# Performance work log

Measured on AMD Instinct MI355X. Metric: run time of the kernel, lower is better.

## Reference

```python
import jax, jax.numpy as jnp
import numpy as np
import math

B, C, H, W = 32, 1024, 32, 32
D = 1024  # d == in_channels == H*W (required by the module's own code)


def _conv1x1(x, w, b):
    # x: (B,C,H,W), w: (out,in), b: (out,)
    return jnp.einsum('bchw,dc->bdhw', x, w) + b[None, :, None, None]


def setup_inputs() -> dict:
    key = jax.random.key(0)
    ks = jax.random.split(key, 20)
    s = 0.02
    d = {'x': jax.random.normal(ks[0], (B, C, H, W), dtype=jnp.float32)}
    names = ['w1', 'w2', 'w3', 'w4', 'w5', 'w6', 'w7']
    for i, n in enumerate(names):
        d[n] = s * jax.random.normal(ks[1 + 2 * i], (D, D), dtype=jnp.float32)
        d['b' + n[1:]] = s * jax.random.normal(ks[2 + 2 * i], (D,), dtype=jnp.float32)
    d['wl'] = s * jax.random.normal(ks[16], (D, D), dtype=jnp.float32)
    d['bl'] = s * jax.random.normal(ks[17], (D,), dtype=jnp.float32)
    return d


def reference(x, w1, b1, w2, b2, w3, b3, w4, b4, w5, b5, w6, b6, w7, b7, wl, bl):
    b, c, h, w = x.shape
    d = w1.shape[0]
    n = h * w
    scale = 1.0 / math.sqrt(d)

    def lin(z):  # Linear(d,d) over the LAST dim (= n = d here)
        return jnp.einsum('bdn,mn->bdm', z, wl) + bl

    # --- attention block 1 ---
    Q1 = _conv1x1(x, w1, b1).reshape(b, d, n)
    K1 = _conv1x1(x, w2, b2).reshape(b, d, n)
    V1 = _conv1x1(x, w3, b3).reshape(b, d, n)
    A1 = jax.nn.softmax(jnp.einsum('bdn,bdm->bnm', Q1, K1) * scale, axis=-1)  # (b,n,n)
    O1 = jnp.einsum('bdm,bnm->bdn', V1, A1)  # V1 @ A1^T -> (b,d,n)
    X1 = O1.reshape(b, d, h, w) + x

    # --- attention block 2 ---
    Q2 = lin(_conv1x1(X1, w5, b5).reshape(b, d, n))
    K2 = lin(_conv1x1(X1, w6, b6).reshape(b, d, n))
    V2 = lin(_conv1x1(X1, w7, b7).reshape(b, d, n))
    A2 = jax.nn.softmax(jnp.einsum('bdn,bdm->bnm', Q2, K2) * scale, axis=-1)  # (b,n,n)
    O2 = jnp.einsum('bnm,bkm->bkn', A2, V2)  # (A2 @ V2^T)^T -> (b,d,n)
    X2 = _conv1x1(O2.reshape(b, d, h, w), w4, b4) + X1
    return X2
```

## Files before the change

### kernel.cpp

```cpp
#include <hip/hip_runtime.h>
#include <hip/hip_bf16.h>
#include <cstdint>

typedef unsigned short u16;
typedef __bf16 bf16x8 __attribute__((ext_vector_type(8)));
typedef float f32x4 __attribute__((ext_vector_type(4)));
typedef unsigned short us8 __attribute__((ext_vector_type(8)));

#define AS1 __attribute__((address_space(1)))
#define AS3 __attribute__((address_space(3)))

__device__ __forceinline__ float b2f(u16 u) {
    union { float f; uint32_t i; } c; c.i = ((uint32_t)u) << 16; return c.f;
}
__device__ __forceinline__ u16 f2b(float f) {
    union { float f; uint32_t i; } c; c.f = f;
    return (u16)((c.i + 0x7fffu + ((c.i >> 16) & 1u)) >> 16);
}

#define BM 256
#define BN 256
#define BK 64
#define GK 1024
#define GN 1024
#define NKT (GK / BK)

#define BAR asm volatile("s_barrier" ::: "memory")

template <typename OutT>
__global__ __launch_bounds__(512, 2) void gemm_nt(
    const u16* __restrict__ A, long long sA,
    const u16* __restrict__ B, long long sB,
    OutT* __restrict__ C, long long sC,
    const float* __restrict__ bias, int biasMode,
    const u16* __restrict__ res, long long sR,
    float scale,
    const float* __restrict__ r1u, const float* __restrict__ r1v)
{
    __shared__ __align__(16) char smem[131072];

    const int t = threadIdx.x;
    const int orig = blockIdx.x;
    const int id2 = (orig & 7) * 64 + (orig >> 3);
    const int bz = id2 >> 4;
    const int by = (id2 >> 2) & 3;
    const int bx = id2 & 3;

    const u16* Ab = A + (size_t)bz * sA + (size_t)(by * BM) * GK;
    const u16* Bb = B + (size_t)bz * sB + (size_t)(bx * BN) * GK;

    const int wave = t >> 6, lane = t & 63;
    const int l16 = lane & 15, quad = lane >> 4;
    const int wr = wave >> 2;
    const int wc = wave & 3;
    const int bq = l16 & 7;

    f32x4 acc[8][4] = {};

    int geoff[2], ldoff[2];
    #pragma unroll
    for (int i = 0; i < 2; ++i) {
        const int c = t + 512 * i;
        const int r = c >> 3, js = c & 7;
        geoff[i] = r * GK + (js ^ (r & 7)) * 8;
        ldoff[i] = c * 16;
    }

    #define STG_A(tile, h)                                                               \
        _Pragma("unroll")                                                                \
        for (int i = 0; i < 2; ++i)                                                      \
            __builtin_amdgcn_global_load_lds(                                            \
                (AS1 const void*)(Ab + (size_t)(h) * 128 * GK + geoff[i] + (tile) * BK), \
                (AS3 void*)(smem + ((tile) & 1) * 65536 + (h) * 16384 + ldoff[i]),       \
                16, 0, 0);
    #define STG_B(tile, h)                                                               \
        _Pragma("unroll")                                                                \
        for (int i = 0; i < 2; ++i)                                                      \
            __builtin_amdgcn_global_load_lds(                                            \
                (AS1 const void*)(Bb + (size_t)(h) * 128 * GK + geoff[i] + (tile) * BK), \
                (AS3 void*)(smem + ((tile) & 1) * 65536 + 32768 + (h) * 16384 + ldoff[i]), \
                16, 0, 0);

    auto ldsA = [&](int p, int mh, int mi, int kk) -> const bf16x8* {
        return (const bf16x8*)(smem + p * 65536 + wr * 16384
            + (mh * 64 + mi * 16 + l16) * 128 + (((kk * 4 + quad) ^ bq) * 16));
    };
    auto ldsB = [&](int p, int nh, int ni, int kk) -> const bf16x8* {
        return (const bf16x8*)(smem + p * 65536 + 32768 + (wc >> 1) * 16384
            + ((wc & 1) * 64 + nh * 32 + ni * 16 + l16) * 128 + (((kk * 4 + quad) ^ bq) * 16));
    };

    auto group = [&](int tile) {
        const int p = tile & 1;
        const bool stA = (tile + 1) < NKT;
        const bool stB = (tile + 2) < NKT;
        bf16x8 af[4][2], b0[2][2], b1[2][2];

        #pragma unroll
        for (int mi = 0; mi < 4; ++mi)
            #pragma unroll
            for (int kk = 0; kk < 2; ++kk)
                af[mi][kk] = *ldsA(p, 0, mi, kk);
        #pragma unroll
        for (int ni = 0; ni < 2; ++ni)
            #pragma unroll
            for (int kk = 0; kk < 2; ++kk)
                b0[ni][kk] = *ldsB(p, 0, ni, kk);
        if (stA) { STG_A(tile + 1, 0) }
        BAR;
        __builtin_amdgcn_s_setprio(1);
        #pragma unroll
        for (int kk = 0; kk < 2; ++kk)
            #pragma unroll
            for (int mi = 0; mi < 4; ++mi)
                #pragma unroll
                for (int ni = 0; ni < 2; ++ni)
                    acc[mi][ni] = __builtin_amdgcn_mfma_f32_16x16x32_bf16(af[mi][kk], b0[ni][kk], acc[mi][ni], 0, 0, 0);
        __builtin_amdgcn_s_setprio(0);
        BAR;

        #pragma unroll
        for (int ni = 0; ni < 2; ++ni)
            #pragma unroll
            for (int kk = 0; kk < 2; ++kk)
                b1[ni][kk] = *ldsB(p, 1, ni, kk);
        if (stA) { STG_A(tile + 1, 1) }
        BAR;
        __builtin_amdgcn_s_setprio(1);
        #pragma unroll
        for (int kk = 0; kk < 2; ++kk)
            #pragma unroll
            for (int mi = 0; mi < 4; ++mi)
                #pragma unroll
                for (int ni = 0; ni < 2; ++ni)
                    acc[mi][2 + ni] = __builtin_amdgcn_mfma_f32_16x16x32_bf16(af[mi][kk], b1[ni][kk], acc[mi][2 + ni], 0, 0, 0);
        __builtin_amdgcn_s_setprio(0);
        BAR;

        #pragma unroll
        for (int mi = 0; mi < 4; ++mi)
            #pragma unroll
            for (int kk = 0; kk < 2; ++kk)
                af[mi][kk] = *ldsA(p, 1, mi, kk);
        if (stB) { STG_B(tile + 2, 0) }
        BAR;
        __builtin_amdgcn_s_setprio(1);
        #pragma unroll
        for (int kk = 0; kk < 2; ++kk)
            #pragma unroll
            for (int mi = 0; mi < 4; ++mi)
                #pragma unroll
                for (int ni = 0; ni < 2; ++ni)
                    acc[4 + mi][2 + ni] = __builtin_amdgcn_mfma_f32_16x16x32_bf16(af[mi][kk], b1[ni][kk], acc[4 + mi][2 + ni], 0, 0, 0);
        __builtin_amdgcn_s_setprio(0);
        BAR;

        if (stB) { STG_B(tile + 2, 1) }
        BAR;
        __builtin_amdgcn_s_setprio(1);
        #pragma unroll
        for (int kk = 0; kk < 2; ++kk)
            #pragma unroll
            for (int mi = 0; mi < 4; ++mi)
                #pragma unroll
                for (int ni = 0; ni < 2; ++ni)
                    acc[4 + mi][ni] = __builtin_amdgcn_mfma_f32_16x16x32_bf16(af[mi][kk], b0[ni][kk], acc[4 + mi][ni], 0, 0, 0);
        __builtin_amdgcn_s_setprio(0);
        if (stB) { asm volatile("s_waitcnt vmcnt(4)" ::: "memory"); }
        else     { asm volatile("s_waitcnt vmcnt(0)" ::: "memory"); }
        BAR;
    };

    STG_A(0, 0) STG_A(0, 1) STG_B(0, 0) STG_B(0, 1) STG_B(1, 0) STG_B(1, 1)
    asm volatile("s_waitcnt vmcnt(4)" ::: "memory");
    BAR;

    #pragma unroll 1
    for (int j = 0; j < NKT / 2; ++j) {
        group(2 * j);
        group(2 * j + 1);
    }

    float* Cs = (float*)smem;
    #pragma unroll
    for (int mh = 0; mh < 2; ++mh) {
        __syncthreads();
        if (wr == mh) {
            #pragma unroll
            for (int mi = 0; mi < 8; ++mi)
                #pragma unroll
                for (int ni = 0; ni < 4; ++ni) {
                    const int col = wc * 64 + ni * 16 + l16;
                    const int jc = col >> 2, cw = col & 3;
                    #pragma unroll
                    for (int r2 = 0; r2 < 4; ++r2) {
                        const int row = mi * 16 + quad * 4 + r2;
                        Cs[row * 256 + ((jc ^ (row & 15)) << 2) + cw] = acc[mi][ni][r2];
                    }
                }
        }
        __syncthreads();

        if constexpr (__is_same(OutT, u16)) {
            #pragma unroll
            for (int i = 0; i < 8; ++i) {
                const int c = t + 512 * i;
                const int lr = c >> 5, cc = c & 31;
                const int sxy = lr & 15;
                const float* s0 = Cs + lr * 256 + (((cc * 2) ^ sxy) << 2);
                const float* s1 = Cs + lr * 256 + (((cc * 2 + 1) ^ sxy) << 2);
                float4 a = *(const float4*)s0;
                float4 b = *(const float4*)s1;
                const int grow = by * BM + mh * 128 + lr;
                const int gcol = bx * BN + cc * 8;
                const float br = (biasMode == 1) ? bias[grow] : 0.0f;
                float v[8] = {a.x, a.y, a.z, a.w, b.x, b.y, b.z, b.w};
                #pragma unroll
                for (int jj = 0; jj < 8; ++jj) v[jj] = v[jj] * scale + br;
                if (biasMode == 2) {
                    float4 c1 = *(const float4*)(bias + gcol);
                    float4 c2 = *(const float4*)(bias + gcol + 4);
                    v[0] += c1.x; v[1] += c1.y; v[2] += c1.z; v[3] += c1.w;
                    v[4] += c2.x; v[5] += c2.y; v[6] += c2.z; v[7] += c2.w;
                }
                if (r1u) {
                    const float u = r1u[grow];
                    float4 c1 = *(const float4*)(r1v + gcol);
                    float4 c2 = *(const float4*)(r1v + gcol + 4);
                    v[0] += u * c1.x; v[1] += u * c1.y; v[2] += u * c1.z; v[3] += u * c1.w;
                    v[4] += u * c2.x; v[5] += u * c2.y; v[6] += u * c2.z; v[7] += u * c2.w;
                }
                if (res) {
                    us8 rv = *(const us8*)(res + (size_t)bz * sR + (size_t)grow * GN + gcol);
                    #pragma unroll
                    for (int jj = 0; jj < 8; ++jj) v[jj] += b2f(rv[jj]);
                }
                us8 o;
                #pragma unroll
                for (int jj = 0; jj < 8; ++jj) o[jj] = f2b(v[jj]);
                *(us8*)((u16*)C + (size_t)bz * sC + (size_t)grow * GN + gcol) = o;
            }
        } else {
            #pragma unroll
            for (int i = 0; i < 16; ++i) {
                const int c = t + 512 * i;
                const int lr = c >> 6, cc4 = c & 63;
                const float* src = Cs + lr * 256 + ((cc4 ^ (lr & 15)) << 2);
                float4 a = *(const float4*)src;
                const int grow = by * BM + mh * 128 + lr;
                const int gcol = bx * BN + cc4 * 4;
                const float br = (biasMode == 1) ? bias[grow] : 0.0f;
                float v[4] = {a.x, a.y, a.z, a.w};
                #pragma unroll
                for (int jj = 0; jj < 4; ++jj) v[jj] = v[jj] * scale + br;
                if (biasMode == 2) {
                    float4 c1 = *(const float4*)(bias + gcol);
                    v[0] += c1.x; v[1] += c1.y; v[2] += c1.z; v[3] += c1.w;
                }
                if (r1u) {
                    const float u = r1u[grow];
                    float4 c1 = *(const float4*)(r1v + gcol);
                    v[0] += u * c1.x; v[1] += u * c1.y; v[2] += u * c1.z; v[3] += u * c1.w;
                }
                if (res) {
                    ushort4 rv = *(const ushort4*)(res + (size_t)bz * sR + (size_t)grow * GN + gcol);
                    v[0] += b2f(rv.x); v[1] += b2f(rv.y); v[2] += b2f(rv.z); v[3] += b2f(rv.w);
                }
                float4 o = {v[0], v[1], v[2], v[3]};
                *(float4*)((float*)C + (size_t)bz * sC + (size_t)grow * GN + gcol) = o;
            }
        }
    }
    #undef STG_A
    #undef STG_B
}

__global__ __launch_bounds__(256) void softmax_rows(u16* __restrict__ S)
{
    const size_t row = blockIdx.x;
    u16* p = S + row * 1024;
    const int t = threadIdx.x;
    ushort4 u = ((const ushort4*)p)[t];
    float v0 = b2f(u.x), v1 = b2f(u.y), v2 = b2f(u.z), v3 = b2f(u.w);

    float m = fmaxf(fmaxf(v0, v1), fmaxf(v2, v3));
    #pragma unroll
    for (int o = 32; o > 0; o >>= 1) m = fmaxf(m, __shfl_xor(m, o, 64));
    __shared__ float red[8];
    const int wave = t >> 6, lane = t & 63;
    if (lane == 0) red[wave] = m;
    __syncthreads();
    m = fmaxf(fmaxf(red[0], red[1]), fmaxf(red[2], red[3]));

    v0 = __expf(v0 - m); v1 = __expf(v1 - m); v2 = __expf(v2 - m); v3 = __expf(v3 - m);
    float s = v0 + v1 + v2 + v3;
    #pragma unroll
    for (int o = 32; o > 0; o >>= 1) s += __shfl_xor(s, o, 64);
    if (lane == 0) red[4 + wave] = s;
    __syncthreads();
    s = red[4] + red[5] + red[6] + red[7];
    const float inv = 1.0f / s;

    u.x = f2b(v0 * inv); u.y = f2b(v1 * inv); u.z = f2b(v2 * inv); u.w = f2b(v3 * inv);
    ((ushort4*)p)[t] = u;
}

__global__ __launch_bounds__(256) void transpose_k(const u16* __restrict__ in, u16* __restrict__ out)
{
    __shared__ u16 tile[64][65];
    const size_t base = (size_t)blockIdx.z * 1024 * 1024;
    const u16* ib = in + base;
    u16* ob = out + base;
    const int t = threadIdx.x;
    const int vc = t & 15;
    const int rr0 = t >> 4;
    const int tr = blockIdx.y * 64, tc = blockIdx.x * 64;

    #pragma unroll
    for (int rr = 0; rr < 4; ++rr) {
        const int row = rr * 16 + rr0;
        ushort4 u = *(const ushort4*)(ib + (size_t)(tr + row) * 1024 + tc + vc * 4);
        tile[row][vc * 4 + 0] = u.x; tile[row][vc * 4 + 1] = u.y;
        tile[row][vc * 4 + 2] = u.z; tile[row][vc * 4 + 3] = u.w;
    }
    __syncthreads();
    #pragma unroll
    for (int rr = 0; rr < 4; ++rr) {
        const int orow = rr * 16 + rr0;
        ushort4 u;
        u.x = tile[vc * 4 + 0][orow]; u.y = tile[vc * 4 + 1][orow];
        u.z = tile[vc * 4 + 2][orow]; u.w = tile[vc * 4 + 3][orow];
        *(ushort4*)(ob + (size_t)(tc + orow) * 1024 + tr + vc * 4) = u;
    }
}

__global__ __launch_bounds__(256) void tconv_k(const float* __restrict__ in, u16* __restrict__ out)
{
    __shared__ float tile[64][65];
    const size_t base = (size_t)blockIdx.z * 1024 * 1024;
    const float* ib = in + base;
    u16* ob = out + base;
    const int t = threadIdx.x;
    const int vc = t & 15;
    const int rr0 = t >> 4;
    const int tr = blockIdx.y * 64, tc = blockIdx.x * 64;

    #pragma unroll
    for (int rr = 0; rr < 4; ++rr) {
        const int row = rr * 16 + rr0;
        float4 u = *(const float4*)(ib + (size_t)(tr + row) * 1024 + tc + vc * 4);
        tile[row][vc * 4 + 0] = u.x; tile[row][vc * 4 + 1] = u.y;
        tile[row][vc * 4 + 2] = u.z; tile[row][vc * 4 + 3] = u.w;
    }
    __syncthreads();
    #pragma unroll
    for (int rr = 0; rr < 4; ++rr) {
        const int orow = rr * 16 + rr0;
        ushort4 u;
        u.x = f2b(tile[vc * 4 + 0][orow]); u.y = f2b(tile[vc * 4 + 1][orow]);
        u.z = f2b(tile[vc * 4 + 2][orow]); u.w = f2b(tile[vc * 4 + 3][orow]);
        *(ushort4*)(ob + (size_t)(tc + orow) * 1024 + tr + vc * 4) = u;
    }
}

struct WPack { const float* in[8]; u16* out[8]; };
__global__ __launch_bounds__(256) void convw_k(WPack p)
{
    const int m = blockIdx.y;
    const int i = (blockIdx.x * 256 + threadIdx.x) * 4;
    float4 v = *(const float4*)(p.in[m] + i);
    ushort4 s;
    s.x = f2b(v.x); s.y = f2b(v.y); s.z = f2b(v.z); s.w = f2b(v.w);
    *(ushort4*)(p.out[m] + i) = s;
}

__global__ __launch_bounds__(256) void rowsum_k(const float* __restrict__ w, float* __restrict__ s)
{
    const int m = blockIdx.x;
    const float* r = w + (size_t)m * 1024;
    const int t = threadIdx.x;
    float4 v = ((const float4*)r)[t];
    float x = v.x + v.y + v.z + v.w;
    #pragma unroll
    for (int o = 32; o > 0; o >>= 1) x += __shfl_xor(x, o, 64);
    __shared__ float red[4];
    if ((t & 63) == 0) red[t >> 6] = x;
    __syncthreads();
    if (t == 0) s[m] = red[0] + red[1] + red[2] + red[3];
}

extern "C" void kernel_launch(void* const* d_in, const int* in_sizes, int n_in,
                              void* d_out, int out_size, void* d_ws, size_t ws_size,
                              hipStream_t stream) {
    const size_t mat = (size_t)32 * 1024 * 1024;
    const long long mm = 1024LL * 1024LL;
    const float sc = 1.0f / 32.0f;

    const float* x  = (const float*)d_in[0];
    const float* w1 = (const float*)d_in[1];  const float* b1 = (const float*)d_in[2];
    const float* w2 = (const float*)d_in[3];  const float* b2 = (const float*)d_in[4];
    const float* w3 = (const float*)d_in[5];  const float* b3 = (const float*)d_in[6];
    const float* w4 = (const float*)d_in[7];  const float* b4 = (const float*)d_in[8];
    const float* w5 = (const float*)d_in[9];  const float* b5 = (const float*)d_in[10];
    const float* w6 = (const float*)d_in[11]; const float* b6 = (const float*)d_in[12];
    const float* w7 = (const float*)d_in[13]; const float* b7 = (const float*)d_in[14];
    const float* wl = (const float*)d_in[15]; const float* bl = (const float*)d_in[16];
    float* out = (float*)d_out;

    u16* A = (u16*)d_ws;
    u16* Bv = A + mat;
    u16* Cv = A + 2 * mat;
    u16* Dv = A + 3 * mat;
    u16* wb = A + 4 * mat;
    u16 *w1b = wb, *w2b = wb + (1<<20), *w3b = wb + 2*(1<<20), *w4b = wb + 3*(1<<20),
        *w5b = wb + 4*(1<<20), *w6b = wb + 5*(1<<20), *w7b = wb + 6*(1<<20), *wlb = wb + 7*(1<<20);
    float* swl = (float*)(wb + 8*(1<<20));
    u16* OutLo = (u16*)d_out;
    u16* OutHi = OutLo + mat;

    WPack wp;
    wp.in[0]=w1; wp.in[1]=w2; wp.in[2]=w3; wp.in[3]=w4; wp.in[4]=w5; wp.in[5]=w6; wp.in[6]=w7; wp.in[7]=wl;
    wp.out[0]=w1b; wp.out[1]=w2b; wp.out[2]=w3b; wp.out[3]=w4b; wp.out[4]=w5b; wp.out[5]=w6b; wp.out[6]=w7b; wp.out[7]=wlb;

    const dim3 blk(256);
    const dim3 blkG(512);
    const dim3 gT(16, 16, 32), gG(512), gS(32 * 1024), gW(1024, 8), gR(1024);
    const float* NUL = nullptr;

    convw_k<<<gW, blk, 0, stream>>>(wp);
    rowsum_k<<<gR, blk, 0, stream>>>(wl, swl);
    tconv_k<<<gT, blk, 0, stream>>>(x, A);

    gemm_nt<u16><<<gG, blkG, 0, stream>>>(A, mm, w1b, 0, Bv, mm, b1, 2, nullptr, 0, 1.0f, NUL, NUL);
    gemm_nt<u16><<<gG, blkG, 0, stream>>>(A, mm, w2b, 0, Cv, mm, b2, 2, nullptr, 0, 1.0f, NUL, NUL);
    gemm_nt<u16><<<gG, blkG, 0, stream>>>(w3b, 0, A, mm, Dv, mm, b3, 1, nullptr, 0, 1.0f, NUL, NUL);
    gemm_nt<u16><<<gG, blkG, 0, stream>>>(Bv, mm, Cv, mm, OutLo, mm, nullptr, 0, nullptr, 0, sc, NUL, NUL);
    softmax_rows<<<gS, blk, 0, stream>>>(OutLo);
    gemm_nt<u16><<<gG, blkG, 0, stream>>>(OutLo, mm, Dv, mm, Bv, mm, nullptr, 0, A, mm, 1.0f, NUL, NUL);
    transpose_k<<<gT, blk, 0, stream>>>(Bv, A);

    gemm_nt<u16><<<gG, blkG, 0, stream>>>(wlb, 0, A, mm, Cv, mm, nullptr, 0, nullptr, 0, 1.0f, NUL, NUL);
    gemm_nt<u16><<<gG, blkG, 0, stream>>>(Cv, mm, w5b, 0, Dv, mm, bl, 1, nullptr, 0, 1.0f, swl, b5);
    gemm_nt<u16><<<gG, blkG, 0, stream>>>(Cv, mm, w6b, 0, OutLo, mm, bl, 1, nullptr, 0, 1.0f, swl, b6);
    gemm_nt<u16><<<gG, blkG, 0, stream>>>(w7b, 0, Cv, mm, OutHi, mm, bl, 2, nullptr, 0, 1.0f, b7, swl);
    gemm_nt<u16><<<gG, blkG, 0, stream>>>(Dv, mm, OutLo, mm, Bv, mm, nullptr, 0, nullptr, 0, sc, NUL, NUL);
    softmax_rows<<<gS, blk, 0, stream>>>(Bv);
    gemm_nt<u16><<<gG, blkG, 0, stream>>>(Bv, mm, OutHi, mm, Cv, mm, nullptr, 0, nullptr, 0, 1.0f, NUL, NUL);
    gemm_nt<float><<<gG, blkG, 0, stream>>>(w4b, 0, Cv, mm, out, mm, b4, 1, A, mm, 1.0f, NUL, NUL);
}
```

Baseline: 1.348 ms.

## Batch independent GEMMs per launch and fuse transpose with fp32 residual epilogue

Makes the GEMM kernel take a small array of operation descriptors indexed by blockIdx.y, so independent GEMMs (Q1/K1, V1/scores, Q2/K2/V2) run in one launch with more blocks to fill the device. The standalone transpose kernel is removed: the O1 GEMM writes its output transposed from shared memory and adds the fp32 input x as residual there. The aim is to cut launch count, tail effects and one full read/write pass over a 64 MB tensor. In exchange the epilogue does strided shared-memory reads, and the mh loop is no longer unrolled. The residual now comes from full-precision x instead of its bf16 copy, which changes numerics slightly.

```diff
diff --git a/kernel.cpp b/kernel.cpp
--- a/kernel.cpp
+++ b/kernel.cpp
@@ -27,16 +27,21 @@
 
 #define BAR asm volatile("s_barrier" ::: "memory")
 
+struct GOp {
+    const u16* A; const u16* B; void* C;
+    long long sA, sB, sC, sR;
+    const float* bias; const u16* res; const float* r1u; const float* r1v;
+    const float* resF;
+    float scale;
+    int biasMode;
+    int transp;
+};
+struct GOps { GOp op[3]; };
+
 template <typename OutT>
-__global__ __launch_bounds__(512, 2) void gemm_nt(
-    const u16* __restrict__ A, long long sA,
-    const u16* __restrict__ B, long long sB,
-    OutT* __restrict__ C, long long sC,
-    const float* __restrict__ bias, int biasMode,
-    const u16* __restrict__ res, long long sR,
-    float scale,
-    const float* __restrict__ r1u, const float* __restrict__ r1v)
-{
+__global__ __launch_bounds__(512, 2) void gemm_nt(GOps P)
+{
+    const GOp& o = P.op[blockIdx.y];
     __shared__ __align__(16) char smem[131072];
 
     const int t = threadIdx.x;
@@ -46,8 +51,8 @@
     const int by = (id2 >> 2) & 3;
     const int bx = id2 & 3;
 
-    const u16* Ab = A + (size_t)bz * sA + (size_t)(by * BM) * GK;
-    const u16* Bb = B + (size_t)bz * sB + (size_t)(bx * BN) * GK;
+    const u16* Ab = o.A + (size_t)bz * o.sA + (size_t)(by * BM) * GK;
+    const u16* Bb = o.B + (size_t)bz * o.sB + (size_t)(bx * BN) * GK;
 
     const int wave = t >> 6, lane = t & 63;
     const int l16 = lane & 15, quad = lane >> 4;
@@ -181,8 +186,9 @@
         group(2 * j + 1);
     }
 
+    const float scale = o.scale;
     float* Cs = (float*)smem;
-    #pragma unroll
+    #pragma unroll 1
     for (int mh = 0; mh < 2; ++mh) {
         __syncthreads();
         if (wr == mh) {
@@ -202,43 +208,71 @@
         __syncthreads();
 
         if constexpr (__is_same(OutT, u16)) {
-            #pragma unroll
-            for (int i = 0; i < 8; ++i) {
-                const int c = t + 512 * i;
-                const int lr = c >> 5, cc = c & 31;
-                const int sxy = lr & 15;
-                const float* s0 = Cs + lr * 256 + (((cc * 2) ^ sxy) << 2);
-                const float* s1 = Cs + lr * 256 + (((cc * 2 + 1) ^ sxy) << 2);
-                float4 a = *(const float4*)s0;
-                float4 b = *(const float4*)s1;
-                const int grow = by * BM + mh * 128 + lr;
-                const int gcol = bx * BN + cc * 8;
-                const float br = (biasMode == 1) ? bias[grow] : 0.0f;
-                float v[8] = {a.x, a.y, a.z, a.w, b.x, b.y, b.z, b.w};
-                #pragma unroll
-                for (int jj = 0; jj < 8; ++jj) v[jj] = v[jj] * scale + br;
-                if (biasMode == 2) {
-                    float4 c1 = *(const float4*)(bias + gcol);
-                    float4 c2 = *(const float4*)(bias + gcol + 4);
-                    v[0] += c1.x; v[1] += c1.y; v[2] += c1.z; v[3] += c1.w;
-                    v[4] += c2.x; v[5] += c2.y; v[6] += c2.z; v[7] += c2.w;
-                }
-                if (r1u) {
-                    const float u = r1u[grow];
-                    float4 c1 = *(const float4*)(r1v + gcol);
-                    float4 c2 = *(const float4*)(r1v + gcol + 4);
-                    v[0] += u * c1.x; v[1] += u * c1.y; v[2] += u * c1.z; v[3] += u * c1.w;
-                    v[4] += u * c2.x; v[5] += u * c2.y; v[6] += u * c2.z; v[7] += u * c2.w;
-                }
-                if (res) {
-                    us8 rv = *(const us8*)(res + (size_t)bz * sR + (size_t)grow * GN + gcol);
+            if (o.transp) {
+                #pragma unroll
+                for (int i = 0; i < 8; ++i) {
+                    const int c = t + 512 * i;
+                    const int j = c >> 4, seg = c & 15;
+                    const int jc = j >> 2, cw = j & 3;
+                    float v[8];
                     #pragma unroll
-                    for (int jj = 0; jj < 8; ++jj) v[jj] += b2f(rv[jj]);
-                }
-                us8 o;
-                #pragma unroll
-                for (int jj = 0; jj < 8; ++jj) o[jj] = f2b(v[jj]);
-                *(us8*)((u16*)C + (size_t)bz * sC + (size_t)grow * GN + gcol) = o;
+                    for (int k = 0; k < 8; ++k) {
+                        const int row = seg * 8 + k;
+                        v[k] = Cs[row * 256 + ((jc ^ (row & 15)) << 2) + cw] * scale;
+                    }
+                    const int grow2 = bx * BN + j;
+                    const int gcol2 = by * BM + mh * 128 + seg * 8;
+                    if (o.resF) {
+                        const float* rp = o.resF + ((size_t)bz << 20) + (size_t)grow2 * 1024 + gcol2;
+                        float4 f1 = *(const float4*)(rp);
+                        float4 f2 = *(const float4*)(rp + 4);
+                        v[0] += f1.x; v[1] += f1.y; v[2] += f1.z; v[3] += f1.w;
+                        v[4] += f2.x; v[5] += f2.y; v[6] += f2.z; v[7] += f2.w;
+                    }
+                    us8 ov;
+                    #pragma unroll
+                    for (int k = 0; k < 8; ++k) ov[k] = f2b(v[k]);
+                    *(us8*)((u16*)o.C + (size_t)bz * o.sC + (size_t)grow2 * GN + gcol2) = ov;
+                }
+            } else {
+                #pragma unroll
+                for (int i = 0; i < 8; ++i) {
+                    const int c = t + 512 * i;
+                    const int lr = c >> 5, cc = c & 31;
+                    const int sxy = lr & 15;
+                    const float* s0 = Cs + lr * 256 + (((cc * 2) ^ sxy) << 2);
+                    const float* s1 = Cs + lr * 256 + (((cc * 2 + 1) ^ sxy) << 2);
+                    float4 a = *(const float4*)s0;
+                    float4 b = *(const float4*)s1;
+                    const int grow = by * BM + mh * 128 + lr;
+                    const int gcol = bx * BN + cc * 8;
+                    const float br = (o.biasMode == 1) ? o.bias[grow] : 0.0f;
+                    float v[8] = {a.x, a.y, a.z, a.w, b.x, b.y, b.z, b.w};
+                    #pragma unroll
+                    for (int jj = 0; jj < 8; ++jj) v[jj] = v[jj] * scale + br;
+                    if (o.biasMode == 2) {
+                        float4 c1 = *(const float4*)(o.bias + gcol);
+                        float4 c2 = *(const float4*)(o.bias + gcol + 4);
+                        v[0] += c1.x; v[1] += c1.y; v[2] += c1.z; v[3] += c1.w;
+                        v[4] += c2.x; v[5] += c2.y; v[6] += c2.z; v[7] += c2.w;
+                    }
+                    if (o.r1u) {
+                        const float u = o.r1u[grow];
+                        float4 c1 = *(const float4*)(o.r1v + gcol);
+                        float4 c2 = *(const float4*)(o.r1v + gcol + 4);
+                        v[0] += u * c1.x; v[1] += u * c1.y; v[2] += u * c1.z; v[3] += u * c1.w;
+                        v[4] += u * c2.x; v[5] += u * c2.y; v[6] += u * c2.z; v[7] += u * c2.w;
+                    }
+                    if (o.res) {
+                        us8 rv = *(const us8*)(o.res + (size_t)bz * o.sR + (size_t)grow * GN + gcol);
+                        #pragma unroll
+                        for (int jj = 0; jj < 8; ++jj) v[jj] += b2f(rv[jj]);
+                    }
+                    us8 ov;
+                    #pragma unroll
+                    for (int jj = 0; jj < 8; ++jj) ov[jj] = f2b(v[jj]);
+                    *(us8*)((u16*)o.C + (size_t)bz * o.sC + (size_t)grow * GN + gcol) = ov;
+                }
             }
         } else {
             #pragma unroll
@@ -249,25 +283,25 @@
                 float4 a = *(const float4*)src;
                 const int grow = by * BM + mh * 128 + lr;
                 const int gcol = bx * BN + cc4 * 4;
-                const float br = (biasMode == 1) ? bias[grow] : 0.0f;
+                const float br = (o.biasMode == 1) ? o.bias[grow] : 0.0f;
                 float v[4] = {a.x, a.y, a.z, a.w};
                 #pragma unroll
                 for (int jj = 0; jj < 4; ++jj) v[jj] = v[jj] * scale + br;
-                if (biasMode == 2) {
-                    float4 c1 = *(const float4*)(bias + gcol);
+                if (o.biasMode == 2) {
+                    float4 c1 = *(const float4*)(o.bias + gcol);
                     v[0] += c1.x; v[1] += c1.y; v[2] += c1.z; v[3] += c1.w;
                 }
-                if (r1u) {
-                    const float u = r1u[grow];
-                    float4 c1 = *(const float4*)(r1v + gcol);
+                if (o.r1u) {
+                    const float u = o.r1u[grow];
+                    float4 c1 = *(const float4*)(o.r1v + gcol);
                     v[0] += u * c1.x; v[1] += u * c1.y; v[2] += u * c1.z; v[3] += u * c1.w;
                 }
-                if (res) {
-                    ushort4 rv = *(const ushort4*)(res + (size_t)bz * sR + (size_t)grow * GN + gcol);
+                if (o.res) {
+                    ushort4 rv = *(const ushort4*)(o.res + (size_t)bz * o.sR + (size_t)grow * GN + gcol);
                     v[0] += b2f(rv.x); v[1] += b2f(rv.y); v[2] += b2f(rv.z); v[3] += b2f(rv.w);
                 }
-                float4 o = {v[0], v[1], v[2], v[3]};
-                *(float4*)((float*)C + (size_t)bz * sC + (size_t)grow * GN + gcol) = o;
+                float4 ov = {v[0], v[1], v[2], v[3]};
+                *(float4*)((float*)o.C + (size_t)bz * o.sC + (size_t)grow * GN + gcol) = ov;
             }
         }
     }
@@ -303,35 +337,6 @@
 
     u.x = f2b(v0 * inv); u.y = f2b(v1 * inv); u.z = f2b(v2 * inv); u.w = f2b(v3 * inv);
     ((ushort4*)p)[t] = u;
-}
-
-__global__ __launch_bounds__(256) void transpose_k(const u16* __restrict__ in, u16* __restrict__ out)
-{
-    __shared__ u16 tile[64][65];
-    const size_t base = (size_t)blockIdx.z * 1024 * 1024;
-    const u16* ib = in + base;
-    u16* ob = out + base;
-    const int t = threadIdx.x;
-    const int vc = t & 15;
-    const int rr0 = t >> 4;
-    const int tr = blockIdx.y * 64, tc = blockIdx.x * 64;
-
-    #pragma unroll
-    for (int rr = 0; rr < 4; ++rr) {
-        const int row = rr * 16 + rr0;
-        ushort4 u = *(const ushort4*)(ib + (size_t)(tr + row) * 1024 + tc + vc * 4);
-        tile[row][vc * 4 + 0] = u.x; tile[row][vc * 4 + 1] = u.y;
-        tile[row][vc * 4 + 2] = u.z; tile[row][vc * 4 + 3] = u.w;
-    }
-    __syncthreads();
-    #pragma unroll
-    for (int rr = 0; rr < 4; ++rr) {
-        const int orow = rr * 16 + rr0;
-        ushort4 u;
-        u.x = tile[vc * 4 + 0][orow]; u.y = tile[vc * 4 + 1][orow];
-        u.z = tile[vc * 4 + 2][orow]; u.w = tile[vc * 4 + 3][orow];
-        *(ushort4*)(ob + (size_t)(tc + orow) * 1024 + tr + vc * 4) = u;
-    }
 }
 
 __global__ __launch_bounds__(256) void tconv_k(const float* __restrict__ in, u16* __restrict__ out)
@@ -387,6 +392,20 @@
     if ((t & 63) == 0) red[t >> 6] = x;
     __syncthreads();
     if (t == 0) s[m] = red[0] + red[1] + red[2] + red[3];
+}
+
+static inline GOp mkop(const u16* A, long long sA, const u16* B, long long sB,
+                       void* C, long long sC,
+                       const float* bias, int bm, const u16* res, long long sR,
+                       float sc, const float* r1u, const float* r1v,
+                       const float* resF, int tr)
+{
+    GOp o;
+    o.A = A; o.B = B; o.C = C;
+    o.sA = sA; o.sB = sB; o.sC = sC; o.sR = sR;
+    o.bias = bias; o.res = res; o.r1u = r1u; o.r1v = r1v; o.resF = resF;
+    o.scale = sc; o.biasMode = bm; o.transp = tr;
+    return o;
 }
 
 extern "C" void kernel_launch(void* const* d_in, const int* in_sizes, int n_in,
@@ -407,11 +426,11 @@
     const float* wl = (const float*)d_in[15]; const float* bl = (const float*)d_in[16];
     float* out = (float*)d_out;
 
-    u16* A = (u16*)d_ws;
-    u16* Bv = A + mat;
-    u16* Cv = A + 2 * mat;
-    u16* Dv = A + 3 * mat;
-    u16* wb = A + 4 * mat;
+    u16* Axt = (u16*)d_ws;
+    u16* Bv = Axt + mat;
+    u16* Cv = Axt + 2 * mat;
+    u16* Dv = Axt + 3 * mat;
+    u16* wb = Axt + 4 * mat;
     u16 *w1b = wb, *w2b = wb + (1<<20), *w3b = wb + 2*(1<<20), *w4b = wb + 3*(1<<20),
         *w5b = wb + 4*(1<<20), *w6b = wb + 5*(1<<20), *w7b = wb + 6*(1<<20), *wlb = wb + 7*(1<<20);
     float* swl = (float*)(wb + 8*(1<<20));
@@ -424,27 +443,37 @@
 
     const dim3 blk(256);
     const dim3 blkG(512);
-    const dim3 gT(16, 16, 32), gG(512), gS(32 * 1024), gW(1024, 8), gR(1024);
+    const dim3 gT(16, 16, 32), gS(32 * 1024), gW(1024, 8), gR(1024);
     const float* NUL = nullptr;
+    const u16* NUS = nullptr;
 
     convw_k<<<gW, blk, 0, stream>>>(wp);
     rowsum_k<<<gR, blk, 0, stream>>>(wl, swl);
-    tconv_k<<<gT, blk, 0, stream>>>(x, A);
-
-    gemm_nt<u16><<<gG, blkG, 0, stream>>>(A, mm, w1b, 0, Bv, mm, b1, 2, nullptr, 0, 1.0f, NUL, NUL);
-    gemm_nt<u16><<<gG, blkG, 0, stream>>>(A, mm, w2b, 0, Cv, mm, b2, 2, nullptr, 0, 1.0f, NUL, NUL);
-    gemm_nt<u16><<<gG, blkG, 0, stream>>>(w3b, 0, A, mm, Dv, mm, b3, 1, nullptr, 0, 1.0f, NUL, NUL);
-    gemm_nt<u16><<<gG, blkG, 0, stream>>>(Bv, mm, Cv, mm, OutLo, mm, nullptr, 0, nullptr, 0, sc, NUL, NUL);
+    tconv_k<<<gT, blk, 0, stream>>>(x, Axt);
+
+    GOps P{};
+
+    P.op[0] = mkop(Axt, mm, w1b, 0, Bv, mm, b1, 2, NUS, 0, 1.0f, NUL, NUL, NUL, 0);
+    P.op[1] = mkop(Axt, mm, w2b, 0, Cv, mm, b2, 2, NUS, 0, 1.0f, NUL, NUL, NUL, 0);
+    gemm_nt<u16><<<dim3(512, 2), blkG, 0, stream>>>(P);
+    P.op[0] = mkop(w3b, 0, Axt, mm, Dv, mm, b3, 1, NUS, 0, 1.0f, NUL, NUL, NUL, 0);
+    P.op[1] = mkop(Bv, mm, Cv, mm, OutLo, mm, NUL, 0, NUS, 0, sc, NUL, NUL, NUL, 0);
+    gemm_nt<u16><<<dim3(512, 2), blkG, 0, stream>>>(P);
     softmax_rows<<<gS, blk, 0, stream>>>(OutLo);
-    gemm_nt<u16><<<gG, blkG, 0, stream>>>(OutLo, mm, Dv, mm, Bv, mm, nullptr, 0, A, mm, 1.0f, NUL, NUL);
-    transpose_k<<<gT, blk, 0, stream>>>(Bv, A);
-
-    gemm_nt<u16><<<gG, blkG, 0, stream>>>(wlb, 0, A, mm, Cv, mm, nullptr, 0, nullptr, 0, 1.0f, NUL, NUL);
-    gemm_nt<u16><<<gG, blkG, 0, stream>>>(Cv, mm, w5b, 0, Dv, mm, bl, 1, nullptr, 0, 1.0f, swl, b5);
-    gemm_nt<u16><<<gG, blkG, 0, stream>>>(Cv, mm, w6b, 0, OutLo, mm, bl, 1, nullptr, 0, 1.0f, swl, b6);
-    gemm_nt<u16><<<gG, blkG, 0, stream>>>(w7b, 0, Cv, mm, OutHi, mm, bl, 2, nullptr, 0, 1.0f, b7, swl);
-    gemm_nt<u16><<<gG, blkG, 0, stream>>>(Dv, mm, OutLo, mm, Bv, mm, nullptr, 0, nullptr, 0, sc, NUL, NUL);
+    P.op[0] = mkop(OutLo, mm, Dv, mm, Axt, mm, NUL, 0, NUS, 0, 1.0f, NUL, NUL, x, 1);
+    gemm_nt<u16><<<dim3(512, 1), blkG, 0, stream>>>(P);
+
+    P.op[0] = mkop(wlb, 0, Axt, mm, Cv, mm, NUL, 0, NUS, 0, 1.0f, NUL, NUL, NUL, 0);
+    gemm_nt<u16><<<dim3(512, 1), blkG, 0, stream>>>(P);
+    P.op[0] = mkop(Cv, mm, w5b, 0, Dv, mm, bl, 1, NUS, 0, 1.0f, swl, b5, NUL, 0);
+    P.op[1] = mkop(Cv, mm, w6b, 0, OutLo, mm, bl, 1, NUS, 0, 1.0f, swl, b6, NUL, 0);
+    P.op[2] = mkop(w7b, 0, Cv, mm, OutHi, mm, bl, 2, NUS, 0, 1.0f, b7, swl, NUL, 0);
+    gemm_nt<u16><<<dim3(512, 3), blkG, 0, stream>>>(P);
+    P.op[0] = mkop(Dv, mm, OutLo, mm, Bv, mm, NUL, 0, NUS, 0, sc, NUL, NUL, NUL, 0);
+    gemm_nt<u16><<<dim3(512, 1), blkG, 0, stream>>>(P);
     softmax_rows<<<gS, blk, 0, stream>>>(Bv);
-    gemm_nt<u16><<<gG, blkG, 0, stream>>>(Bv, mm, OutHi, mm, Cv, mm, nullptr, 0, nullptr, 0, 1.0f, NUL, NUL);
-    gemm_nt<float><<<gG, blkG, 0, stream>>>(w4b, 0, Cv, mm, out, mm, b4, 1, A, mm, 1.0f, NUL, NUL);
-}
+    P.op[0] = mkop(Bv, mm, OutHi, mm, Cv, mm, NUL, 0, NUS, 0, 1.0f, NUL, NUL, NUL, 0);
+    gemm_nt<u16><<<dim3(512, 1), blkG, 0, stream>>>(P);
+    P.op[0] = mkop(w4b, 0, Cv, mm, out, mm, b4, 1, Axt, mm, 1.0f, NUL, NUL, NUL, 0);
+    gemm_nt<float><<<dim3(512, 1), blkG, 0, stream>>>(P);
+}
```

Measured after the change: 2.654 ms. +97.0%, slower.

## Fold w7 projection into w4 via precomputed W4·W7 product, reassociating final GEMMs

Applied to the files above, without the earlier changes.

Precomputes W47 = W4·W7 (plus the rank-1 bias correction vectors rowsum(W4) and W4·b7) once per call, and reassociates the tail of block 2. The value projection V2 is never materialised: W47 is applied to the linear output, and the result is multiplied by the attention matrix in the final GEMM with residual. This removes one full batched 1024^3 GEMM from the activation path at the cost of a small weight-only GEMM, a transpose, two matvec kernels, and extra rank-1 epilogue terms. The bf16 rounding points shift, so the numerics change slightly. The block-swizzle now scales with gridDim so the 16-block weight GEMM indexes correctly.

```diff
diff --git a/kernel.cpp b/kernel.cpp
--- a/kernel.cpp
+++ b/kernel.cpp
@@ -35,13 +35,15 @@
     const float* __restrict__ bias, int biasMode,
     const u16* __restrict__ res, long long sR,
     float scale,
-    const float* __restrict__ r1u, const float* __restrict__ r1v)
+    const float* __restrict__ r1u, const float* __restrict__ r1v,
+    const float* __restrict__ r2u, const float* __restrict__ r2v)
 {
     __shared__ __align__(16) char smem[131072];
 
     const int t = threadIdx.x;
     const int orig = blockIdx.x;
-    const int id2 = (orig & 7) * 64 + (orig >> 3);
+    const int cpx = gridDim.x >> 3;
+    const int id2 = (orig & 7) * cpx + (orig >> 3);
     const int bz = id2 >> 4;
     const int by = (id2 >> 2) & 3;
     const int bx = id2 & 3;
@@ -230,6 +232,13 @@
                     v[0] += u * c1.x; v[1] += u * c1.y; v[2] += u * c1.z; v[3] += u * c1.w;
                     v[4] += u * c2.x; v[5] += u * c2.y; v[6] += u * c2.z; v[7] += u * c2.w;
                 }
+                if (r2u) {
+                    const float u = r2u[grow];
+                    float4 c1 = *(const float4*)(r2v + gcol);
+                    float4 c2 = *(const float4*)(r2v + gcol + 4);
+                    v[0] += u * c1.x; v[1] += u * c1.y; v[2] += u * c1.z; v[3] += u * c1.w;
+                    v[4] += u * c2.x; v[5] += u * c2.y; v[6] += u * c2.z; v[7] += u * c2.w;
+                }
                 if (res) {
                     us8 rv = *(const us8*)(res + (size_t)bz * sR + (size_t)grow * GN + gcol);
                     #pragma unroll
@@ -262,6 +271,11 @@
                     float4 c1 = *(const float4*)(r1v + gcol);
                     v[0] += u * c1.x; v[1] += u * c1.y; v[2] += u * c1.z; v[3] += u * c1.w;
                 }
+                if (r2u) {
+                    const float u = r2u[grow];
+                    float4 c1 = *(const float4*)(r2v + gcol);
+                    v[0] += u * c1.x; v[1] += u * c1.y; v[2] += u * c1.z; v[3] += u * c1.w;
+                }
                 if (res) {
                     ushort4 rv = *(const ushort4*)(res + (size_t)bz * sR + (size_t)grow * GN + gcol);
                     v[0] += b2f(rv.x); v[1] += b2f(rv.y); v[2] += b2f(rv.z); v[3] += b2f(rv.w);
@@ -387,6 +401,24 @@
     if ((t & 63) == 0) red[t >> 6] = x;
     __syncthreads();
     if (t == 0) s[m] = red[0] + red[1] + red[2] + red[3];
+}
+
+__global__ __launch_bounds__(256) void matvec_k(const float* __restrict__ w,
+                                                const float* __restrict__ vvec,
+                                                float* __restrict__ outv)
+{
+    const int m = blockIdx.x;
+    const float* r = w + (size_t)m * 1024;
+    const int t = threadIdx.x;
+    float4 a = ((const float4*)r)[t];
+    float4 b = ((const float4*)vvec)[t];
+    float x = a.x * b.x + a.y * b.y + a.z * b.z + a.w * b.w;
+    #pragma unroll
+    for (int o = 32; o > 0; o >>= 1) x += __shfl_xor(x, o, 64);
+    __shared__ float red[4];
+    if ((t & 63) == 0) red[t >> 6] = x;
+    __syncthreads();
+    if (t == 0) outv[m] = red[0] + red[1] + red[2] + red[3];
 }
 
 extern "C" void kernel_launch(void* const* d_in, const int* in_sizes, int n_in,
@@ -414,9 +446,13 @@
     u16* wb = A + 4 * mat;
     u16 *w1b = wb, *w2b = wb + (1<<20), *w3b = wb + 2*(1<<20), *w4b = wb + 3*(1<<20),
         *w5b = wb + 4*(1<<20), *w6b = wb + 5*(1<<20), *w7b = wb + 6*(1<<20), *wlb = wb + 7*(1<<20);
-    float* swl = (float*)(wb + 8*(1<<20));
+    u16* extra = wb + 8 * (1<<20);
+    float* swl   = (float*)extra;
+    float* sw4   = swl + 1024;
+    float* w4b7v = swl + 2048;
+    u16* w7tb = extra + 8192;
+    u16* W47b = w7tb + (1<<20);
     u16* OutLo = (u16*)d_out;
-    u16* OutHi = OutLo + mat;
 
     WPack wp;
     wp.in[0]=w1; wp.in[1]=w2; wp.in[2]=w3; wp.in[3]=w4; wp.in[4]=w5; wp.in[5]=w6; wp.in[6]=w7; wp.in[7]=wl;
@@ -424,27 +460,32 @@
 
     const dim3 blk(256);
     const dim3 blkG(512);
-    const dim3 gT(16, 16, 32), gG(512), gS(32 * 1024), gW(1024, 8), gR(1024);
+    const dim3 gG(512), gG1(16);
+    const dim3 gT(16, 16, 32), gT1(16, 16, 1), gS(32 * 1024), gW(1024, 8), gR(1024);
     const float* NUL = nullptr;
 
     convw_k<<<gW, blk, 0, stream>>>(wp);
     rowsum_k<<<gR, blk, 0, stream>>>(wl, swl);
+    rowsum_k<<<gR, blk, 0, stream>>>(w4, sw4);
+    matvec_k<<<gR, blk, 0, stream>>>(w4, b7, w4b7v);
+    transpose_k<<<gT1, blk, 0, stream>>>(w7b, w7tb);
+    gemm_nt<u16><<<gG1, blkG, 0, stream>>>(w4b, 0, w7tb, 0, W47b, 0,
+        NUL, 0, nullptr, 0, 1.0f, NUL, NUL, NUL, NUL);
     tconv_k<<<gT, blk, 0, stream>>>(x, A);
 
-    gemm_nt<u16><<<gG, blkG, 0, stream>>>(A, mm, w1b, 0, Bv, mm, b1, 2, nullptr, 0, 1.0f, NUL, NUL);
-    gemm_nt<u16><<<gG, blkG, 0, stream>>>(A, mm, w2b, 0, Cv, mm, b2, 2, nullptr, 0, 1.0f, NUL, NUL);
-    gemm_nt<u16><<<gG, blkG, 0, stream>>>(w3b, 0, A, mm, Dv, mm, b3, 1, nullptr, 0, 1.0f, NUL, NUL);
-    gemm_nt<u16><<<gG, blkG, 0, stream>>>(Bv, mm, Cv, mm, OutLo, mm, nullptr, 0, nullptr, 0, sc, NUL, NUL);
+    gemm_nt<u16><<<gG, blkG, 0, stream>>>(A, mm, w1b, 0, Bv, mm, b1, 2, nullptr, 0, 1.0f, NUL, NUL, NUL, NUL);
+    gemm_nt<u16><<<gG, blkG, 0, stream>>>(A, mm, w2b, 0, Cv, mm, b2, 2, nullptr, 0, 1.0f, NUL, NUL, NUL, NUL);
+    gemm_nt<u16><<<gG, blkG, 0, stream>>>(w3b, 0, A, mm, Dv, mm, b3, 1, nullptr, 0, 1.0f, NUL, NUL, NUL, NUL);
+    gemm_nt<u16><<<gG, blkG, 0, stream>>>(Bv, mm, Cv, mm, OutLo, mm, NUL, 0, nullptr, 0, sc, NUL, NUL, NUL, NUL);
     softmax_rows<<<gS, blk, 0, stream>>>(OutLo);
-    gemm_nt<u16><<<gG, blkG, 0, stream>>>(OutLo, mm, Dv, mm, Bv, mm, nullptr, 0, A, mm, 1.0f, NUL, NUL);
+    gemm_nt<u16><<<gG, blkG, 0, stream>>>(OutLo, mm, Dv, mm, Bv, mm, NUL, 0, A, mm, 1.0f, NUL, NUL, NUL, NUL);
     transpose_k<<<gT, blk, 0, stream>>>(Bv, A);
 
-    gemm_nt<u16><<<gG, blkG, 0, stream>>>(wlb, 0, A, mm, Cv, mm, nullptr, 0, nullptr, 0, 1.0f, NUL, NUL);
-    gemm_nt<u16><<<gG, blkG, 0, stream>>>(Cv, mm, w5b, 0, Dv, mm, bl, 1, nullptr, 0, 1.0f, swl, b5);
-    gemm_nt<u16><<<gG, blkG, 0, stream>>>(Cv, mm, w6b, 0, OutLo, mm, bl, 1, nullptr, 0, 1.0f, swl, b6);
-    gemm_nt<u16><<<gG, blkG, 0, stream>>>(w7b, 0, Cv, mm, OutHi, mm, bl, 2, nullptr, 0, 1.0f, b7, swl);
-    gemm_nt<u16><<<gG, blkG, 0, stream>>>(Dv, mm, OutLo, mm, Bv, mm, nullptr, 0, nullptr, 0, sc, NUL, NUL);
+    gemm_nt<u16><<<gG, blkG, 0, stream>>>(wlb, 0, A, mm, Cv, mm, NUL, 0, nullptr, 0, 1.0f, NUL, NUL, NUL, NUL);
+    gemm_nt<u16><<<gG, blkG, 0, stream>>>(Cv, mm, w5b, 0, Dv, mm, bl, 1, nullptr, 0, 1.0f, swl, b5, NUL, NUL);
+    gemm_nt<u16><<<gG, blkG, 0, stream>>>(Cv, mm, w6b, 0, OutLo, mm, bl, 1, nullptr, 0, 1.0f, swl, b6, NUL, NUL);
+    gemm_nt<u16><<<gG, blkG, 0, stream>>>(Dv, mm, OutLo, mm, Bv, mm, NUL, 0, nullptr, 0, sc, NUL, NUL, NUL, NUL);
     softmax_rows<<<gS, blk, 0, stream>>>(Bv);
-    gemm_nt<u16><<<gG, blkG, 0, stream>>>(Bv, mm, OutHi, mm, Cv, mm, nullptr, 0, nullptr, 0, 1.0f, NUL, NUL);
-    gemm_nt<float><<<gG, blkG, 0, stream>>>(w4b, 0, Cv, mm, out, mm, b4, 1, A, mm, 1.0f, NUL, NUL);
-}
+    gemm_nt<u16><<<gG, blkG, 0, stream>>>(W47b, 0, Cv, mm, Dv, mm, NUL, 0, nullptr, 0, 1.0f, sw4, bl, w4b7v, swl);
+    gemm_nt<float><<<gG, blkG, 0, stream>>>(Dv, mm, Bv, mm, out, mm, b4, 1, A, mm, 1.0f, NUL, NUL, NUL, NUL);
+}
```

After: 1.295 ms. 1.04x faster.
